# Performance work log

Hardware: AMD Instinct MI355X
Metric: run time of the kernel (lower is better)

## Reference

```python
import jax, jax.numpy as jnp
import numpy as np

B, N, K = 8, 4096, 5


def setup_inputs() -> dict:
    key = jax.random.key(0)
    ks = jax.random.split(key, 24)
    s = 0.05
    inp = {
        'pointcloud': jax.random.normal(ks[0], (B, 3, N, 1), jnp.float32),
        # local 1x1 conv stack (bias-free) + BN affine params (eval mode, stats=identity)
        'conv_w1': jax.random.normal(ks[1], (64, 3), jnp.float32) * s,
        'bn1_g': jnp.ones((64,), jnp.float32), 'bn1_b': jnp.zeros((64,), jnp.float32),
        'conv_w2': jax.random.normal(ks[2], (64, 64), jnp.float32) * s,
        'bn2_g': jnp.ones((64,), jnp.float32), 'bn2_b': jnp.zeros((64,), jnp.float32),
        'conv_w3': jax.random.normal(ks[3], (64, 64), jnp.float32) * s,
        'bn3_g': jnp.ones((64,), jnp.float32), 'bn3_b': jnp.zeros((64,), jnp.float32),
        'conv_w4': jax.random.normal(ks[4], (128, 64), jnp.float32) * s,
        'bn4_g': jnp.ones((128,), jnp.float32), 'bn4_b': jnp.zeros((128,), jnp.float32),
        # GCN layers
        'gc1_w': jax.random.normal(ks[5], (128, 128), jnp.float32) * s,
        'gc1_b': jnp.zeros((128,), jnp.float32),
        'gc2_w': jax.random.normal(ks[6], (128, 128), jnp.float32) * s,
        'gc2_b': jnp.zeros((128,), jnp.float32),
        'gc3_w': jax.random.normal(ks[7], (128, 256), jnp.float32) * s,
        'gc3_b': jnp.zeros((256,), jnp.float32),
        # MLP head
        'fc1_w': jax.random.normal(ks[8], (512, 256), jnp.float32) * s,
        'bnf1_g': jnp.ones((512,), jnp.float32), 'bnf1_b': jnp.zeros((512,), jnp.float32),
        'fc2_w': jax.random.normal(ks[9], (256, 512), jnp.float32) * s,
        'bnf2_g': jnp.ones((256,), jnp.float32), 'bnf2_b': jnp.zeros((256,), jnp.float32),
        'fc3_w': jax.random.normal(ks[10], (128, 256), jnp.float32) * s,
        'fc3_b': jnp.zeros((128,), jnp.float32),
    }
    return inp


def _cbr(h, w, g, b):
    # 1x1 conv (per-point linear) + BatchNorm(eval, identity stats) + ReLU
    return jax.nn.relu((h @ w.T) * g + b)


def reference(pointcloud, conv_w1, bn1_g, bn1_b, conv_w2, bn2_g, bn2_b,
              conv_w3, bn3_g, bn3_b, conv_w4, bn4_g, bn4_b,
              gc1_w, gc1_b, gc2_w, gc2_b, gc3_w, gc3_b,
              fc1_w, bnf1_g, bnf1_b, fc2_w, bnf2_g, bnf2_b, fc3_w, fc3_b):
    pts = pointcloud[..., 0]                       # [B,3,N]
    b, _, n = pts.shape

    # ---- LocalOperation: sort points by distance to centroid, gather ----
    centroid = pts.mean(axis=2, keepdims=True)     # [B,3,1]
    d_cent = ((pts - centroid) ** 2).sum(axis=1)   # [B,N]
    order = jnp.argsort(d_cent, axis=-1)           # [B,N]
    x = jnp.take_along_axis(pts, order[:, None, :], axis=2)  # [B,3,N]

    h = x.transpose(0, 2, 1)                       # [B,N,3]
    h = _cbr(h, conv_w1, bn1_g, bn1_b)             # [B,N,64]
    h = _cbr(h, conv_w2, bn2_g, bn2_b)
    h = _cbr(h, conv_w3, bn3_g, bn3_b)
    h = _cbr(h, conv_w4, bn4_g, bn4_b)             # [B,N,128]
    feat = h.reshape(b * n, 128)                   # node features

    # ---- KNN graph (k=5, within each cloud, self included like KDTree) ----
    sq = (pts ** 2).sum(axis=1)                                        # [B,N]
    d2 = sq[:, :, None] + sq[:, None, :] - 2.0 * jnp.einsum('bcn,bcm->bnm', pts, pts)
    _, nbr = jax.lax.top_k(-d2, K)                                     # [B,N,K]
    offsets = (jnp.arange(b) * n)[:, None, None]
    src = (nbr + offsets).reshape(-1)                                  # [B*N*K]
    dst = jnp.broadcast_to(jnp.arange(b * n).reshape(b, n, 1), (b, n, K)).reshape(-1)

    num_nodes = b * n
    ones = jnp.ones_like(src, jnp.float32)
    deg_out = jax.ops.segment_sum(ones, src, num_segments=num_nodes)
    deg_in = jax.ops.segment_sum(ones, dst, num_segments=num_nodes)
    norm_out = jax.lax.rsqrt(jnp.maximum(deg_out, 1.0))
    norm_in = jax.lax.rsqrt(jnp.maximum(deg_in, 1.0))

    def gcn(hh, w, bias):
        hw = (hh @ w) * norm_out[:, None]          # [BN,F] pre-normed features
        msg = hw[src]                              # gather
        agg = jax.ops.segment_sum(msg, dst, num_segments=num_nodes)  # scatter-add
        return agg * norm_in[:, None] + bias

    g = jax.nn.relu(gcn(feat, gc1_w, gc1_b))       # [BN,128]
    g = jax.nn.relu(gcn(g, gc2_w, gc2_b))          # [BN,128]
    g = gcn(g, gc3_w, gc3_b)                       # [BN,256]

    # ---- head (BN eval, dropout eval = identity) ----
    z = jax.nn.relu((g @ fc1_w.T) * bnf1_g + bnf1_b)   # [BN,512]
    z = jax.nn.relu((z @ fc2_w.T) * bnf2_g + bnf2_b)   # [BN,256]
    pooled = z.max(axis=0)                             # [256] global max over nodes
    out = pooled @ fc3_w.T + fc3_b                     # [128]
    return out
```

## Files before the change

kernel.cpp:

```cpp
#include <hip/hip_runtime.h>
#include <math.h>
#include <float.h>

#define NB 8
#define NP 4096
#define BN_ (NB*NP)
#define KNN 5
#define JCH 512
#define NJC (NP/JCH)
#define SENT 64

typedef unsigned short u16;
typedef __attribute__((ext_vector_type(8))) __bf16 bf16x8;
typedef __attribute__((ext_vector_type(4))) float f32x4;

__device__ __forceinline__ u16 f2bf(float x){
  unsigned u = __float_as_uint(x);
  u += 0x7fff + ((u>>16)&1);
  return (u16)(u>>16);
}
__device__ __forceinline__ float bf2f(u16 h){ return __uint_as_float(((unsigned)h)<<16); }


__global__ void k_centroid(const float* __restrict__ pc, float* __restrict__ dcent,
                           int* __restrict__ rankb) {
  int b = blockIdx.x, tid = threadIdx.x;
  const float* px = pc + (size_t)b*3*NP;
  const float* py = px + NP;
  const float* pz = py + NP;
  double sx=0, sy=0, sz=0;
  for (int n = tid; n < NP; n += 256) { sx += px[n]; sy += py[n]; sz += pz[n]; }
  __shared__ double rx[256], ry[256], rz[256];
  rx[tid]=sx; ry[tid]=sy; rz[tid]=sz;
  __syncthreads();
  for (int s = 128; s > 0; s >>= 1) {
    if (tid < s) { rx[tid]+=rx[tid+s]; ry[tid]+=ry[tid+s]; rz[tid]+=rz[tid+s]; }
    __syncthreads();
  }
  __shared__ float cxs, cys, czs;
  if (tid == 0) {
    cxs = (float)(rx[0]/NP); cys = (float)(ry[0]/NP); czs = (float)(rz[0]/NP);
  }
  __syncthreads();
  float cx = cxs, cy = cys, cz = czs;
  for (int n = tid; n < NP; n += 256) {
    float dx = __fsub_rn(px[n], cx);
    float dy = __fsub_rn(py[n], cy);
    float dz = __fsub_rn(pz[n], cz);
    float d = __fadd_rn(__fadd_rn(__fmul_rn(dx,dx), __fmul_rn(dy,dy)), __fmul_rn(dz,dz));
    dcent[b*NP + n] = d;
    rankb[b*NP + n] = 0;
  }
}

__global__ void __launch_bounds__(256) k_rank_part(const float* __restrict__ dcent,
                                                   int* __restrict__ rank) {
  int jc = blockIdx.x, ic = blockIdx.y, b = blockIdx.z;
  __shared__ float d[JCH];
  int j0 = jc*JCH;
  for (int n = threadIdx.x; n < JCH; n += 256) d[n] = dcent[b*NP + j0 + n];
  __syncthreads();
  int i = ic*256 + threadIdx.x;
  float di = dcent[b*NP + i];
  int cnt = 0;
  #pragma unroll 8
  for (int n = 0; n < JCH; ++n) {
    float dj = d[n];
    cnt += (dj < di) || (dj == di && (j0 + n) < i);
  }
  atomicAdd(&rank[b*NP + i], cnt);
}

__global__ void k_scatprep(const float* __restrict__ pc, const int* __restrict__ rank,
                           const float* __restrict__ dcent,
                           int* __restrict__ ord, float4* __restrict__ srt,
                           float* __restrict__ rcv, int* __restrict__ deg) {
  int idx = blockIdx.x*256 + threadIdx.x;
  int b = idx >> 12, i = idx & (NP-1);
  int r = rank[idx];
  ord[b*NP + r] = i;
  const float* base = pc + (size_t)b*3*NP;
  float x = base[i], y = base[NP+i], z = base[2*NP+i];
  float sq = __fadd_rn(__fadd_rn(__fmul_rn(x,x), __fmul_rn(y,y)), __fmul_rn(z,z));
  float4 v; v.x=x; v.y=y; v.z=z; v.w=sq;
  srt[b*NP + r] = v;
  rcv[b*NP + r] = sqrtf(dcent[idx]);
  deg[idx] = 0;
}

#define INS(dist, q) \
  if (dist < b4) { \
    if (dist < b3) { b4=b3; r4=r3; \
      if (dist < b2) { b3=b2; r3=r2; \
        if (dist < b1) { b2=b1; r2=r1; \
          if (dist < b0) { b1=b0; r1=r0; b0=dist; r0=(q); } \
          else { b1=dist; r1=(q); } \
        } else { b2=dist; r2=(q); } \
      } else { b3=dist; r3=(q); } \
    } else { b4=dist; r4=(q); } \
  }

__global__ void __launch_bounds__(512) k_knn_ann4(const float4* __restrict__ srt,
                                                  const float* __restrict__ rc,
                                                  const int* __restrict__ ord,
                                                  int* __restrict__ nbr,
                                                  int* __restrict__ deg) {
  __shared__ float4 tile[NP + 2*SENT];
  int b = blockIdx.x >> 6;
  int blk = blockIdx.x & 63;
  int gbase = b*NP;
  for (int t = threadIdx.x; t < NP + 2*SENT; t += 512) {
    int q = t - SENT;
    if ((unsigned)q < NP) tile[t] = srt[gbase + q];
    else { float4 s4; s4.x=0.f; s4.y=0.f; s4.z=0.f; s4.w=1e30f; tile[t] = s4; }
  }
  __syncthreads();

  const int lane = threadIdx.x & 63;
  const int wv   = threadIdx.x >> 6;
  const int grp  = lane >> 3;
  const int sub  = lane & 7;
  const int s_i  = blk*64 + wv*8 + grp;

  float4 p = tile[SENT + s_i];
  float xi=p.x, yi=p.y, zi=p.z, sqi=p.w;
  float ri = rc[gbase + s_i];

  const bool is_hi = (sub < 4);
  const int step = is_hi ? 4 : -4;
  const int jdead = is_hi ? (NP + 7) : (-36);
  int j = is_hi ? (s_i + sub) : (s_i - 1 - (sub - 4));
  bool alive = ((unsigned)j < NP);
  if (!alive) j = jdead;

  float b0=FLT_MAX, b1=FLT_MAX, b2=FLT_MAX, b3=FLT_MAX, b4=FLT_MAX;
  int r0=0, r1=0, r2=0, r3=0, r4=0;

  while (__ballot(alive)) {
    float4 jp[8];
    #pragma unroll
    for (int t = 0; t < 8; ++t) jp[t] = tile[SENT + j + step*t];
    #pragma unroll
    for (int t = 0; t < 8; ++t) {
      float dot = __fadd_rn(__fadd_rn(__fmul_rn(xi,jp[t].x), __fmul_rn(yi,jp[t].y)), __fmul_rn(zi,jp[t].z));
      float dist = __fsub_rn(__fadd_rn(sqi, jp[t].w), __fmul_rn(2.0f, dot));
      if (__ballot(dist < b4)) { INS(dist, j + step*t) }
    }
    float bm = b4;
    bm = fminf(bm, __shfl_xor(bm, 1));
    bm = fminf(bm, __shfl_xor(bm, 2));
    bm = fminf(bm, __shfl_xor(bm, 4));
    float T = bm*1.0002f + 1e-9f;
    int qe = j + step*7;
    qe = qe < 0 ? 0 : (qe > NP-1 ? NP-1 : qe);
    float dr = fabsf(ri - rc[gbase + qe]);
    bool nextin = ((unsigned)(j + step*8) < NP);
    alive = alive && nextin && (__fmul_rn(dr,dr) < T);
    j = alive ? (j + step*8) : jdead;
  }

  #pragma unroll
  for (int m = 1; m <= 4; m <<= 1) {
    float c0=__shfl_xor(b0,m), c1=__shfl_xor(b1,m), c2=__shfl_xor(b2,m),
          c3=__shfl_xor(b3,m), c4=__shfl_xor(b4,m);
    int   s0=__shfl_xor(r0,m), s1=__shfl_xor(r1,m), s2=__shfl_xor(r2,m),
          s3=__shfl_xor(r3,m), s4=__shfl_xor(r4,m);
    if (c0 < b4) { INS(c0, s0)
      if (c1 < b4) { INS(c1, s1)
        if (c2 < b4) { INS(c2, s2)
          if (c3 < b4) { INS(c3, s3)
            if (c4 < b4) { INS(c4, s4) }
          }
        }
      }
    }
  }

  if (sub == 0) {
    int oi = ord[gbase + s_i];
    int node = gbase + oi;
    int nb = node*KNN;
    int o0 = gbase + ord[gbase+r0], o1 = gbase + ord[gbase+r1], o2 = gbase + ord[gbase+r2];
    int o3 = gbase + ord[gbase+r3], o4 = gbase + ord[gbase+r4];
    nbr[nb+0]=o0; nbr[nb+1]=o1; nbr[nb+2]=o2; nbr[nb+3]=o3; nbr[nb+4]=o4;
    atomicAdd(&deg[o0],1); atomicAdd(&deg[o1],1); atomicAdd(&deg[o2],1);
    atomicAdd(&deg[o3],1); atomicAdd(&deg[o4],1);
  }
}

__global__ void k_cvt_all(const float* __restrict__ w2, const float* __restrict__ w3,
                          const float* __restrict__ w4, const float* __restrict__ gc1,
                          const float* __restrict__ gc2, const float* __restrict__ gc3,
                          const float* __restrict__ fc1, const float* __restrict__ fc2,
                          u16* o2, u16* o3, u16* o4, u16* og1, u16* og2, u16* og3,
                          u16* of1, u16* of2) {
  int i = blockIdx.x*256 + threadIdx.x;
  if (i < 4096) { o2[i] = f2bf(w2[i]); return; } i -= 4096;
  if (i < 4096) { o3[i] = f2bf(w3[i]); return; } i -= 4096;
  if (i < 8192) { o4[i] = f2bf(w4[i]); return; } i -= 8192;
  if (i < 16384) { int n=i>>7, k=i&127; og1[i] = f2bf(gc1[k*128+n]); return; } i -= 16384;
  if (i < 16384) { int n=i>>7, k=i&127; og2[i] = f2bf(gc2[k*128+n]); return; } i -= 16384;
  if (i < 32768) { int n=i>>7, k=i&127; og3[i] = f2bf(gc3[k*256+n]); return; } i -= 32768;
  if (i < 131072) { of1[i] = f2bf(fc1[i]); return; } i -= 131072;
  if (i < 131072) { of2[i] = f2bf(fc2[i]); }
}

__global__ void __launch_bounds__(256) k_convstack(
    const float* __restrict__ pc, const int* __restrict__ ord,
    const float* __restrict__ w1, const float* __restrict__ g1, const float* __restrict__ b1,
    const u16* __restrict__ wb2, const float* __restrict__ g2, const float* __restrict__ b2,
    const u16* __restrict__ wb3, const float* __restrict__ g3, const float* __restrict__ b3,
    const u16* __restrict__ wb4, const float* __restrict__ g4, const float* __restrict__ b4,
    u16* __restrict__ feat, float* __restrict__ pooled) {
  __shared__ float xs[128], ys[128], zs[128];
  __shared__ u16 hA[128*64];
  __shared__ u16 hB[128*64];
  __shared__ u16 wbuf[128*64];
  const int tid = threadIdx.x;
  const int m0 = blockIdx.x * 128;
  const int b = m0 >> 12;
  if (blockIdx.x == 0) pooled[tid] = 0.0f;
  if (tid < 128) {
    int j = ord[m0 + tid];
    const float* base = pc + (size_t)b*3*NP;
    xs[tid] = base[j]; ys[tid] = base[NP + j]; zs[tid] = base[2*NP + j];
  }
  #pragma unroll
  for (int it = 0; it < 2; ++it) {
    int t = tid + it*256;
    int row = t >> 3, lc = t & 7;
    uint4 v = *(const uint4*)(wb2 + ((size_t)row*64 + lc*8));
    *(uint4*)&wbuf[row*64 + ((lc ^ (row&7))*8)] = v;
  }
  __syncthreads();

  for (int idx = tid; idx < 128*64; idx += 256) {
    int n = idx >> 6, o = idx & 63;
    float x = xs[n], y = ys[n], z = zs[n];
    float acc = x*w1[o*3+0] + y*w1[o*3+1] + z*w1[o*3+2];
    float v = fmaxf(acc*g1[o] + b1[o], 0.0f);
    hA[n*64 + (((o>>3) ^ (n&7))*8) + (o&7)] = f2bf(v);
  }
  __syncthreads();

  const int w = tid >> 6, l = tid & 63;
  const int wm = w & 1, wn = w >> 1;
  const int fm = l & 15, fk = l >> 4;

  {
    f32x4 acc[4][2];
    #pragma unroll
    for (int i=0;i<4;++i) { acc[i][0]=(f32x4){0,0,0,0}; acc[i][1]=(f32x4){0,0,0,0}; }
    #pragma unroll
    for (int ks=0; ks<2; ++ks){
      bf16x8 af[4], bfr[2];
      #pragma unroll
      for (int mf=0; mf<4; ++mf){
        int row = wm*64 + mf*16 + fm; int ck = ks*4 + fk;
        af[mf] = *(const bf16x8*)&hA[row*64 + ((ck ^ (row&7))*8)];
      }
      #pragma unroll
      for (int nf=0; nf<2; ++nf){
        int row = wn*32 + nf*16 + fm; int ck = ks*4 + fk;
        bfr[nf] = *(const bf16x8*)&wbuf[row*64 + ((ck ^ (row&7))*8)];
      }
      #pragma unroll
      for (int mf=0; mf<4; ++mf)
        #pragma unroll
        for (int nf=0; nf<2; ++nf)
          acc[mf][nf] = __builtin_amdgcn_mfma_f32_16x16x32_bf16(af[mf], bfr[nf], acc[mf][nf], 0, 0, 0);
    }
    #pragma unroll
    for (int mf=0; mf<4; ++mf)
      #pragma unroll
      for (int r=0;r<4;++r){
        int row = wm*64 + mf*16 + fk*4 + r;
        #pragma unroll
        for (int nf=0;nf<2;++nf){
          int col = wn*32 + nf*16 + fm;
          float v = fmaxf(acc[mf][nf][r]*g2[col] + b2[col], 0.f);
          hB[row*64 + (((col>>3) ^ (row&7))*8) + (col&7)] = f2bf(v);
        }
      }
  }
  __syncthreads();
  #pragma unroll
  for (int it = 0; it < 2; ++it) {
    int t = tid + it*256;
    int row = t >> 3, lc = t & 7;
    uint4 v = *(const uint4*)(wb3 + ((size_t)row*64 + lc*8));
    *(uint4*)&wbuf[row*64 + ((lc ^ (row&7))*8)] = v;
  }
  __syncthreads();

  {
    f32x4 acc[4][2];
    #pragma unroll
    for (int i=0;i<4;++i) { acc[i][0]=(f32x4){0,0,0,0}; acc[i][1]=(f32x4){0,0,0,0}; }
    #pragma unroll
    for (int ks=0; ks<2; ++ks){
      bf16x8 af[4], bfr[2];
      #pragma unroll
      for (int mf=0; mf<4; ++mf){
        int row = wm*64 + mf*16 + fm; int ck = ks*4 + fk;
        af[mf] = *(const bf16x8*)&hB[row*64 + ((ck ^ (row&7))*8)];
      }
      #pragma unroll
      for (int nf=0; nf<2; ++nf){
        int row = wn*32 + nf*16 + fm; int ck = ks*4 + fk;
        bfr[nf] = *(const bf16x8*)&wbuf[row*64 + ((ck ^ (row&7))*8)];
      }
      #pragma unroll
      for (int mf=0; mf<4; ++mf)
        #pragma unroll
        for (int nf=0; nf<2; ++nf)
          acc[mf][nf] = __builtin_amdgcn_mfma_f32_16x16x32_bf16(af[mf], bfr[nf], acc[mf][nf], 0, 0, 0);
    }
    #pragma unroll
    for (int mf=0; mf<4; ++mf)
      #pragma unroll
      for (int r=0;r<4;++r){
        int row = wm*64 + mf*16 + fk*4 + r;
        #pragma unroll
        for (int nf=0;nf<2;++nf){
          int col = wn*32 + nf*16 + fm;
          float v = fmaxf(acc[mf][nf][r]*g3[col] + b3[col], 0.f);
          hA[row*64 + (((col>>3) ^ (row&7))*8) + (col&7)] = f2bf(v);
        }
      }
  }
  __syncthreads();
  #pragma unroll
  for (int it = 0; it < 4; ++it) {
    int t = tid + it*256;
    int row = t >> 3, lc = t & 7;
    uint4 v = *(const uint4*)(wb4 + ((size_t)row*64 + lc*8));
    *(uint4*)&wbuf[row*64 + ((lc ^ (row&7))*8)] = v;
  }
  __syncthreads();

  {
    f32x4 acc[4][4];
    #pragma unroll
    for (int i=0;i<4;++i)
      #pragma unroll
      for (int jn=0;jn<4;++jn) acc[i][jn]=(f32x4){0,0,0,0};
    #pragma unroll
    for (int ks=0; ks<2; ++ks){
      bf16x8 af[4], bfr[4];
      #pragma unroll
      for (int mf=0; mf<4; ++mf){
        int row = wm*64 + mf*16 + fm; int ck = ks*4 + fk;
        af[mf] = *(const bf16x8*)&hA[row*64 + ((ck ^ (row&7))*8)];
      }
      #pragma unroll
      for (int nf=0; nf<4; ++nf){
        int row = wn*64 + nf*16 + fm; int ck = ks*4 + fk;
        bfr[nf] = *(const bf16x8*)&wbuf[row*64 + ((ck ^ (row&7))*8)];
      }
      #pragma unroll
      for (int mf=0; mf<4; ++mf)
        #pragma unroll
        for (int nf=0; nf<4; ++nf)
          acc[mf][nf] = __builtin_amdgcn_mfma_f32_16x16x32_bf16(af[mf], bfr[nf], acc[mf][nf], 0, 0, 0);
    }
    #pragma unroll
    for (int mf=0; mf<4; ++mf)
      #pragma unroll
      for (int r=0;r<4;++r){
        int row = m0 + wm*64 + mf*16 + fk*4 + r;
        #pragma unroll
        for (int nf=0;nf<4;++nf){
          int col = wn*64 + nf*16 + fm;
          float v = fmaxf(acc[mf][nf][r]*g4[col] + b4[col], 0.f);
          feat[(size_t)row*128 + col] = f2bf(v);
        }
      }
  }
}

template<int BNT>
__global__ __launch_bounds__(256) void gemm_bf16(
    const u16* __restrict__ A, const u16* __restrict__ W,
    const float* __restrict__ gamma, const float* __restrict__ beta,
    const int* __restrict__ degp, void* __restrict__ Cout,
    int K, int Nc, int mode) {
  constexpr int NF = BNT/32;
  __shared__ u16 As[128*64];
  __shared__ u16 Bs[BNT*64];
  const int tid = threadIdx.x;
  const int w = tid >> 6, l = tid & 63;
  const int m0 = blockIdx.x*128, n0 = blockIdx.y*BNT;
  const int wm = w & 1, wn = w >> 1;
  const int lr = l >> 3;
  const int lc = l & 7;
  const int fm = l & 15, fk = l >> 4;

  f32x4 acc[4][NF];
  #pragma unroll
  for (int i=0;i<4;++i)
    #pragma unroll
    for (int j=0;j<NF;++j) acc[i][j] = (f32x4){0.f,0.f,0.f,0.f};

  for (int k0 = 0; k0 < K; k0 += 64) {
    #pragma unroll
    for (int t=0;t<4;++t){
      int row = (w*4 + t)*8 + lr;
      uint4 v = *(const uint4*)(A + ((size_t)(m0+row)*K + k0 + lc*8));
      *(uint4*)&As[row*64 + ((lc ^ (row&7))*8)] = v;
    }
    #pragma unroll
    for (int t=0;t<NF;++t){
      int row = (w*NF + t)*8 + lr;
      uint4 v = *(const uint4*)(W + ((size_t)(n0+row)*K + k0 + lc*8));
      *(uint4*)&Bs[row*64 + ((lc ^ (row&7))*8)] = v;
    }
    __syncthreads();
    #pragma unroll
    for (int ks=0; ks<2; ++ks){
      bf16x8 af[4], bfr[NF];
      #pragma unroll
      for (int mf=0; mf<4; ++mf){
        int row = wm*64 + mf*16 + fm;
        int ck = ks*4 + fk;
        af[mf] = *(const bf16x8*)&As[row*64 + ((ck ^ (row&7))*8)];
      }
      #pragma unroll
      for (int nf=0; nf<NF; ++nf){
        int row = wn*(BNT/2) + nf*16 + fm;
        int ck = ks*4 + fk;
        bfr[nf] = *(const bf16x8*)&Bs[row*64 + ((ck ^ (row&7))*8)];
      }
      #pragma unroll
      for (int mf=0; mf<4; ++mf)
        #pragma unroll
        for (int nf=0; nf<NF; ++nf)
          acc[mf][nf] = __builtin_amdgcn_mfma_f32_16x16x32_bf16(af[mf], bfr[nf], acc[mf][nf], 0, 0, 0);
    }
    __syncthreads();
  }

  const int col_base = n0 + wn*(BNT/2);
  if (mode == 1) {
    u16* C = (u16*)Cout;
    #pragma unroll
    for (int mf=0; mf<4; ++mf){
      #pragma unroll
      for (int r=0;r<4;++r){
        int row = m0 + wm*64 + mf*16 + fk*4 + r;
        int d = degp[row]; if (d < 1) d = 1;
        float rs = 1.0f / sqrtf((float)d);
        #pragma unroll
        for (int nf=0;nf<NF;++nf){
          int col = col_base + nf*16 + fm;
          C[(size_t)row*Nc + col] = f2bf(acc[mf][nf][r]*rs);
        }
      }
    }
  } else if (mode == 3) {
    unsigned int* pool = (unsigned int*)Cout;
    float gv[NF], bv[NF], cm[NF];
    #pragma unroll
    for (int nf=0;nf<NF;++nf){
      int col = col_base + nf*16 + fm;
      gv[nf] = gamma[col]; bv[nf] = beta[col];
      cm[nf] = 0.0f;
    }
    #pragma unroll
    for (int mf=0; mf<4; ++mf)
      #pragma unroll
      for (int r=0;r<4;++r)
        #pragma unroll
        for (int nf=0;nf<NF;++nf){
          float v = fmaxf(acc[mf][nf][r]*gv[nf] + bv[nf], 0.f);
          cm[nf] = fmaxf(cm[nf], v);
        }
    #pragma unroll
    for (int nf=0;nf<NF;++nf){
      float m = cm[nf];
      m = fmaxf(m, __shfl_xor(m, 16));
      m = fmaxf(m, __shfl_xor(m, 32));
      if (fk == 0)
        atomicMax(&pool[col_base + nf*16 + fm], __float_as_uint(m));
    }
  } else {
    float gv[NF], bv[NF];
    #pragma unroll
    for (int nf=0;nf<NF;++nf){
      int col = col_base + nf*16 + fm;
      gv[nf] = gamma[col]; bv[nf] = beta[col];
    }
    #pragma unroll
    for (int mf=0; mf<4; ++mf){
      #pragma unroll
      for (int r=0;r<4;++r){
        int row = m0 + wm*64 + mf*16 + fk*4 + r;
        #pragma unroll
        for (int nf=0;nf<NF;++nf){
          int col = col_base + nf*16 + fm;
          float v = fmaxf(acc[mf][nf][r]*gv[nf] + bv[nf], 0.f);
          ((u16*)Cout)[(size_t)row*Nc + col] = f2bf(v);
        }
      }
    }
  }
}

__global__ void k_agg_bf(const u16* __restrict__ hw, const int* __restrict__ nbr,
                         const float* __restrict__ bias, u16* __restrict__ outp,
                         int F, int do_relu) {
  int per = F >> 3;
  int gid = blockIdx.x*256 + threadIdx.x;
  int i = gid / per;
  int f = (gid - i*per) * 8;
  const int* nb = nbr + i*KNN;
  float s[8] = {0,0,0,0,0,0,0,0};
  #pragma unroll
  for (int k = 0; k < KNN; ++k) {
    uint4 v = *(const uint4*)(hw + (size_t)nb[k]*F + f);
    const u16* h = (const u16*)&v;
    #pragma unroll
    for (int j=0;j<8;++j) s[j] += bf2f(h[j]);
  }
  const float ninv = 0.44721359549995793f;
  u16 o[8];
  #pragma unroll
  for (int j=0;j<8;++j){
    float v = s[j]*ninv + bias[f+j];
    if (do_relu) v = fmaxf(v, 0.f);
    o[j] = f2bf(v);
  }
  *(uint4*)&outp[(size_t)i*F + f] = *(const uint4*)o;
}

__global__ void k_fc3(const float* __restrict__ pooled, const float* __restrict__ w,
                      const float* __restrict__ bias, float* __restrict__ outp) {
  __shared__ float p[256];
  int tid = threadIdx.x;
  p[tid] = pooled[tid];
  p[tid + 128] = pooled[tid + 128];
  __syncthreads();
  float s = 0.0f;
  for (int i = 0; i < 256; ++i) s = fmaf(w[tid*256 + i], p[i], s);
  outp[tid] = s + bias[tid];
}

extern "C" void kernel_launch(void* const* d_in, const int* in_sizes, int n_in,
                              void* d_out, int out_size, void* d_ws, size_t ws_size,
                              hipStream_t stream) {
  const float* pc   = (const float*)d_in[0];
  const float* w1   = (const float*)d_in[1];
  const float* g1   = (const float*)d_in[2];
  const float* b1   = (const float*)d_in[3];
  const float* w2   = (const float*)d_in[4];
  const float* g2   = (const float*)d_in[5];
  const float* b2   = (const float*)d_in[6];
  const float* w3   = (const float*)d_in[7];
  const float* g3   = (const float*)d_in[8];
  const float* b3   = (const float*)d_in[9];
  const float* w4   = (const float*)d_in[10];
  const float* g4   = (const float*)d_in[11];
  const float* b4   = (const float*)d_in[12];
  const float* gc1w = (const float*)d_in[13];
  const float* gc1b = (const float*)d_in[14];
  const float* gc2w = (const float*)d_in[15];
  const float* gc2b = (const float*)d_in[16];
  const float* gc3w = (const float*)d_in[17];
  const float* gc3b = (const float*)d_in[18];
  const float* fc1w = (const float*)d_in[19];
  const float* f1g  = (const float*)d_in[20];
  const float* f1b  = (const float*)d_in[21];
  const float* fc2w = (const float*)d_in[22];
  const float* f2g  = (const float*)d_in[23];
  const float* f2b  = (const float*)d_in[24];
  const float* fc3w = (const float*)d_in[25];
  const float* fc3b = (const float*)d_in[26];
  float* outp = (float*)d_out;

  char* wsb = (char*)d_ws;
  size_t off = 0;
  auto alloc = [&](size_t bytes) -> void* {
    void* p = wsb + off;
    off += (bytes + 255) & ~(size_t)255;
    return p;
  };
  int*   ord    = (int*)  alloc((size_t)BN_*4);
  int*   deg    = (int*)  alloc((size_t)BN_*4);
  int*   rankb  = (int*)  alloc((size_t)BN_*4);
  int*   nbr    = (int*)  alloc((size_t)BN_*KNN*4);
  float* dcent  = (float*)alloc((size_t)BN_*4);
  float* pooled = (float*)alloc(256*4);
  float4* srt   = (float4*)alloc((size_t)BN_*16);
  float* rc     = (float*)alloc((size_t)BN_*4);
  u16* wb2   = (u16*)alloc(64*64*2);
  u16* wb3   = (u16*)alloc(64*64*2);
  u16* wb4   = (u16*)alloc(128*64*2);
  u16* wgc1  = (u16*)alloc(128*128*2);
  u16* wgc2  = (u16*)alloc(128*128*2);
  u16* wgc3  = (u16*)alloc(256*128*2);
  u16* wfc1  = (u16*)alloc(512*256*2);
  u16* wfc2  = (u16*)alloc(256*512*2);
  u16* feat = (u16*)alloc((size_t)BN_*128*2);
  u16* hw   = (u16*)alloc((size_t)BN_*256*2);
  u16* gb1  = (u16*)alloc((size_t)BN_*128*2);
  u16* g3b  = (u16*)alloc((size_t)BN_*256*2);
  u16* z1   = (u16*)alloc((size_t)BN_*512*2);

  k_cvt_all<<<1344, 256, 0, stream>>>(w2, w3, w4, gc1w, gc2w, gc3w, fc1w, fc2w,
                                      wb2, wb3, wb4, wgc1, wgc2, wgc3, wfc1, wfc2);

  k_centroid<<<NB, 256, 0, stream>>>(pc, dcent, rankb);
  k_rank_part<<<dim3(NJC, NP/256, NB), 256, 0, stream>>>(dcent, rankb);
  k_scatprep<<<BN_/256, 256, 0, stream>>>(pc, rankb, dcent, ord, srt, rc, deg);
  k_knn_ann4<<<NB*64, 512, 0, stream>>>(srt, rc, ord, nbr, deg);

  k_convstack<<<BN_/128, 256, 0, stream>>>(pc, ord, w1, g1, b1,
                                           wb2, g2, b2, wb3, g3, b3, wb4, g4, b4,
                                           feat, pooled);

  gemm_bf16<128><<<dim3(BN_/128, 1), 256, 0, stream>>>(feat, wgc1, nullptr, nullptr, deg, hw, 128, 128, 1);
  k_agg_bf<<<(BN_*16)/256, 256, 0, stream>>>(hw, nbr, gc1b, gb1, 128, 1);
  gemm_bf16<128><<<dim3(BN_/128, 1), 256, 0, stream>>>(gb1, wgc2, nullptr, nullptr, deg, hw, 128, 128, 1);
  k_agg_bf<<<(BN_*16)/256, 256, 0, stream>>>(hw, nbr, gc2b, feat, 128, 1);
  gemm_bf16<128><<<dim3(BN_/128, 2), 256, 0, stream>>>(feat, wgc3, nullptr, nullptr, deg, hw, 128, 256, 1);
  k_agg_bf<<<(BN_*32)/256, 256, 0, stream>>>(hw, nbr, gc3b, g3b, 256, 0);

  gemm_bf16<128><<<dim3(BN_/128, 4), 256, 0, stream>>>(g3b, wfc1, f1g, f1b, nullptr, z1, 256, 512, 0);
  gemm_bf16<128><<<dim3(BN_/128, 2), 256, 0, stream>>>(z1, wfc2, f2g, f2b, nullptr, pooled, 512, 256, 3);
  k_fc3<<<1, 128, 0, stream>>>(pooled, fc3w, fc3b, outp);
}
```

Before: 338.6 us.

## Window shared tile in kNN search, widen lane groups, vectorize rank loop

```diff
diff --git a/kernel.cpp b/kernel.cpp
--- a/kernel.cpp
+++ b/kernel.cpp
@@ -8,7 +8,8 @@
 #define KNN 5
 #define JCH 512
 #define NJC (NP/JCH)
-#define SENT 64
+#define TW 2432
+#define TE (TW + 128)
 
 typedef unsigned short u16;
 typedef __attribute__((ext_vector_type(8))) __bf16 bf16x8;
@@ -56,17 +57,20 @@
 __global__ void __launch_bounds__(256) k_rank_part(const float* __restrict__ dcent,
                                                    int* __restrict__ rank) {
   int jc = blockIdx.x, ic = blockIdx.y, b = blockIdx.z;
-  __shared__ float d[JCH];
+  __shared__ __attribute__((aligned(16))) float d[JCH];
   int j0 = jc*JCH;
   for (int n = threadIdx.x; n < JCH; n += 256) d[n] = dcent[b*NP + j0 + n];
   __syncthreads();
   int i = ic*256 + threadIdx.x;
   float di = dcent[b*NP + i];
   int cnt = 0;
-  #pragma unroll 8
-  for (int n = 0; n < JCH; ++n) {
-    float dj = d[n];
-    cnt += (dj < di) || (dj == di && (j0 + n) < i);
+  #pragma unroll 4
+  for (int n = 0; n < JCH; n += 4) {
+    float4 dv = *(const float4*)&d[n];
+    cnt += (dv.x < di) || (dv.x == di && (j0 + n + 0) < i);
+    cnt += (dv.y < di) || (dv.y == di && (j0 + n + 1) < i);
+    cnt += (dv.z < di) || (dv.z == di && (j0 + n + 2) < i);
+    cnt += (dv.w < di) || (dv.w == di && (j0 + n + 3) < i);
   }
   atomicAdd(&rank[b*NP + i], cnt);
 }
@@ -105,31 +109,35 @@
                                                   const int* __restrict__ ord,
                                                   int* __restrict__ nbr,
                                                   int* __restrict__ deg) {
-  __shared__ float4 tile[NP + 2*SENT];
-  int b = blockIdx.x >> 6;
-  int blk = blockIdx.x & 63;
-  int gbase = b*NP;
-  for (int t = threadIdx.x; t < NP + 2*SENT; t += 512) {
-    int q = t - SENT;
-    if ((unsigned)q < NP) tile[t] = srt[gbase + q];
+  __shared__ float4 tile[TE];
+  const int b = blockIdx.x >> 7;
+  const int blk = blockIdx.x & 127;
+  const int gbase = b*NP;
+  const int base = blk*32;
+  const int tlo = base - 1200;
+  const int thi = tlo + TW;
+  for (int t = threadIdx.x; t < TE; t += 512) {
+    int q = tlo + t - 64;
+    bool real = ((unsigned)(t - 64) < (unsigned)TW) && ((unsigned)q < NP);
+    if (real) tile[t] = srt[gbase + q];
     else { float4 s4; s4.x=0.f; s4.y=0.f; s4.z=0.f; s4.w=1e30f; tile[t] = s4; }
   }
   __syncthreads();
 
   const int lane = threadIdx.x & 63;
   const int wv   = threadIdx.x >> 6;
-  const int grp  = lane >> 3;
-  const int sub  = lane & 7;
-  const int s_i  = blk*64 + wv*8 + grp;
-
-  float4 p = tile[SENT + s_i];
+  const int grp  = lane >> 4;
+  const int sub  = lane & 15;
+  const int s_i  = base + wv*4 + grp;
+
+  float4 p = tile[s_i - tlo + 64];
   float xi=p.x, yi=p.y, zi=p.z, sqi=p.w;
   float ri = rc[gbase + s_i];
 
-  const bool is_hi = (sub < 4);
-  const int step = is_hi ? 4 : -4;
-  const int jdead = is_hi ? (NP + 7) : (-36);
-  int j = is_hi ? (s_i + sub) : (s_i - 1 - (sub - 4));
+  const bool is_hi = (sub < 8);
+  const int step = is_hi ? 8 : -8;
+  const int jdead = is_hi ? (thi + 7) : (tlo - 8);
+  int j = is_hi ? (s_i + sub) : (s_i - 1 - (sub - 8));
   bool alive = ((unsigned)j < NP);
   if (!alive) j = jdead;
 
@@ -137,19 +145,39 @@
   int r0=0, r1=0, r2=0, r3=0, r4=0;
 
   while (__ballot(alive)) {
-    float4 jp[8];
-    #pragma unroll
-    for (int t = 0; t < 8; ++t) jp[t] = tile[SENT + j + step*t];
-    #pragma unroll
-    for (int t = 0; t < 8; ++t) {
-      float dot = __fadd_rn(__fadd_rn(__fmul_rn(xi,jp[t].x), __fmul_rn(yi,jp[t].y)), __fmul_rn(zi,jp[t].z));
-      float dist = __fsub_rn(__fadd_rn(sqi, jp[t].w), __fmul_rn(2.0f, dot));
-      if (__ballot(dist < b4)) { INS(dist, j + step*t) }
+    bool fast = (!alive) || (is_hi ? (j + 56 < thi) : (j - 56 >= tlo));
+    if (__ballot(!fast) == 0ULL) {
+      float4 jp[8];
+      #pragma unroll
+      for (int t = 0; t < 8; ++t) jp[t] = tile[j - tlo + 64 + step*t];
+      #pragma unroll
+      for (int t = 0; t < 8; ++t) {
+        float dot = __fadd_rn(__fadd_rn(__fmul_rn(xi,jp[t].x), __fmul_rn(yi,jp[t].y)), __fmul_rn(zi,jp[t].z));
+        float dist = __fsub_rn(__fadd_rn(sqi, jp[t].w), __fmul_rn(2.0f, dot));
+        if (__ballot(dist < b4)) { INS(dist, j + step*t) }
+      }
+    } else {
+      #pragma unroll
+      for (int t = 0; t < 8; ++t) {
+        int jt = j + step*t;
+        float4 q4;
+        if ((unsigned)(jt - tlo) < (unsigned)TW) {
+          q4 = tile[jt - tlo + 64];
+        } else {
+          int qc = jt < 0 ? 0 : (jt > NP-1 ? NP-1 : jt);
+          q4 = srt[gbase + qc];
+          if (!(alive && (unsigned)jt < NP)) q4.w = 1e30f;
+        }
+        float dot = __fadd_rn(__fadd_rn(__fmul_rn(xi,q4.x), __fmul_rn(yi,q4.y)), __fmul_rn(zi,q4.z));
+        float dist = __fsub_rn(__fadd_rn(sqi, q4.w), __fmul_rn(2.0f, dot));
+        if (__ballot(dist < b4)) { INS(dist, jt) }
+      }
     }
     float bm = b4;
     bm = fminf(bm, __shfl_xor(bm, 1));
     bm = fminf(bm, __shfl_xor(bm, 2));
     bm = fminf(bm, __shfl_xor(bm, 4));
+    bm = fminf(bm, __shfl_xor(bm, 8));
     float T = bm*1.0002f + 1e-9f;
     int qe = j + step*7;
     qe = qe < 0 ? 0 : (qe > NP-1 ? NP-1 : qe);
@@ -160,7 +188,7 @@
   }
 
   #pragma unroll
-  for (int m = 1; m <= 4; m <<= 1) {
+  for (int m = 1; m <= 8; m <<= 1) {
     float c0=__shfl_xor(b0,m), c1=__shfl_xor(b1,m), c2=__shfl_xor(b2,m),
           c3=__shfl_xor(b3,m), c4=__shfl_xor(b4,m);
     int   s0=__shfl_xor(r0,m), s1=__shfl_xor(r1,m), s2=__shfl_xor(r2,m),
@@ -612,7 +640,7 @@
   k_centroid<<<NB, 256, 0, stream>>>(pc, dcent, rankb);
   k_rank_part<<<dim3(NJC, NP/256, NB), 256, 0, stream>>>(dcent, rankb);
   k_scatprep<<<BN_/256, 256, 0, stream>>>(pc, rankb, dcent, ord, srt, rc, deg);
-  k_knn_ann4<<<NB*64, 512, 0, stream>>>(srt, rc, ord, nbr, deg);
+  k_knn_ann4<<<NB*128, 512, 0, stream>>>(srt, rc, ord, nbr, deg);
 
   k_convstack<<<BN_/128, 256, 0, stream>>>(pc, ord, w1, g1, b1,
                                            wb2, g2, b2, wb3, g3, b3, wb4, g4, b4,
```

Result: slower. 354.6 us (+4.7%).
